# Optimization experiments

Measured on AMD Instinct MI355X. Metric: run time of the kernel, lower is better.

## Reference

```python
import jax, jax.numpy as jnp
import numpy as np

TAIL_BOUND = 3.0
MIN_BIN_W = 1e-3
MIN_BIN_H = 1e-3
MIN_DERIV = 1e-3


def _rq_spline_fwd(x, uw, uh, us):
    # unconstrained rational-quadratic spline (Durkan et al., 'linear' tails)
    # x: [N, C]; uw, uh: [C, B]; us: [C, B-1]
    C, B = uw.shape
    dt = x.dtype
    inside = (x >= -TAIL_BOUND) & (x <= TAIL_BOUND)
    xc = jnp.clip(x, -TAIL_BOUND, TAIL_BOUND)

    widths = MIN_BIN_W + (1.0 - MIN_BIN_W * B) * jax.nn.softmax(uw, axis=-1)
    cumw = jnp.concatenate([jnp.zeros((C, 1), dt), jnp.cumsum(widths, -1)], -1)
    cumw = 2.0 * TAIL_BOUND * cumw - TAIL_BOUND
    cumw = cumw.at[:, 0].set(-TAIL_BOUND).at[:, -1].set(TAIL_BOUND)
    widths = cumw[:, 1:] - cumw[:, :-1]

    heights = MIN_BIN_H + (1.0 - MIN_BIN_H * B) * jax.nn.softmax(uh, axis=-1)
    cumh = jnp.concatenate([jnp.zeros((C, 1), dt), jnp.cumsum(heights, -1)], -1)
    cumh = 2.0 * TAIL_BOUND * cumh - TAIL_BOUND
    cumh = cumh.at[:, 0].set(-TAIL_BOUND).at[:, -1].set(TAIL_BOUND)
    heights = cumh[:, 1:] - cumh[:, :-1]

    # boundary derivative logits -> softplus(const) = 1 - MIN_DERIV
    const = float(np.log(np.expm1(1.0 - MIN_DERIV)))
    ud = jnp.concatenate([jnp.full((C, 1), const, dt), us,
                          jnp.full((C, 1), const, dt)], -1)
    derivs = MIN_DERIV + jax.nn.softplus(ud)  # [C, B+1]

    # searchsorted on bin x-edges (eps shift on last edge, as in reference impl)
    edges = cumw.at[:, -1].add(1e-6)
    idx = jnp.clip(jnp.sum(xc[:, :, None] >= edges[None, :, :], -1) - 1, 0, B - 1)  # [N, C]

    ci = jnp.arange(C)[None, :]
    xk = cumw[ci, idx]
    wk = widths[ci, idx]
    yk = cumh[ci, idx]
    hk = heights[ci, idx]
    dk = derivs[ci, idx]
    dk1 = derivs[ci, idx + 1]
    delta = hk / wk

    theta = (xc - xk) / wk
    t1m = theta * (1.0 - theta)
    num = hk * (delta * theta * theta + dk * t1m)
    den = delta + (dk + dk1 - 2.0 * delta) * t1m
    y = yk + num / den
    dnum = delta * delta * (dk1 * theta * theta + 2.0 * delta * t1m
                            + dk * (1.0 - theta) * (1.0 - theta))
    logdet = jnp.log(dnum) - 2.0 * jnp.log(den)

    # identity (log-det 0) outside the interval
    return jnp.where(inside, y, x), jnp.where(inside, logdet, jnp.zeros_like(logdet))


def setup_inputs() -> dict:
    key = jax.random.key(0)
    ks = jax.random.split(key, 6)
    N, L, C, B = 1000000, 8, 8, 32
    return {
        "x": jax.random.normal(ks[0], (N,), jnp.float32),
        "w": jax.random.normal(ks[1], (L, C, B), jnp.float32),
        "h": jax.random.normal(ks[2], (L, C, B), jnp.float32),
        "s": jax.random.normal(ks[3], (L, C, B - 1), jnp.float32),
        "bias": jax.random.normal(ks[4], (L + 1, C), jnp.float32),
        "log_scale": jax.random.normal(ks[5], (L + 1, C), jnp.float32),
    }


def reference(x, w, h, s, bias, log_scale):
    L, C = w.shape[0], w.shape[1]
    z = jnp.broadcast_to(x[:, None], (x.shape[0], C))
    log_j = jnp.zeros_like(z)
    for step in range(L):
        z = (z - bias[step]) * jnp.exp(-log_scale[step])
        z, ld = _rq_spline_fwd(z, w[step], h[step], s[step])
        log_j = log_j + ld - log_scale[step]
    z = (z - bias[L]) * jnp.exp(-log_scale[L])
    return z, log_j - log_scale[L]
```

## Files before the change

kernel.cpp:

```cpp
#include <hip/hip_runtime.h>
#include <hip/hip_bf16.h>


#define TB 3.0f
#define NB 32
#define NC 8
#define NL 8
#define LN2 0.69314718055994530942f

#define GX0 -6.5f
#define GX1 6.5f
#define TZ 0.5f
#define TL 0.5f

#define PT_FLOATS (64 * 99)
#define GP_FLOATS (PT_FLOATS + 72 + 72 + 8)
#define GP_BYTES  (GP_FLOATS * 4)
#define TAB_OFF   26112
#define CAP 256

__device__ __forceinline__ float softplusf(float v) {
    return fmaxf(v, 0.f) + log1pf(expf(-fabsf(v)));
}

__device__ __forceinline__ unsigned short f2h(float f) {
    _Float16 h = (_Float16)f;
    unsigned short u;
    __builtin_memcpy(&u, &h, 2);
    return u;
}
__device__ __forceinline__ float h2f(unsigned short u) {
    _Float16 h;
    __builtin_memcpy(&h, &u, 2);
    return (float)h;
}

__device__ __forceinline__ int bsearch32(const float* __restrict__ E, float xc) {
    int i = (xc >= E[16]) ? 16 : 0;
    i += (xc >= E[i + 8]) ? 8 : 0;
    i += (xc >= E[i + 4]) ? 4 : 0;
    i += (xc >= E[i + 2]) ? 2 : 0;
    i += (xc >= E[i + 1]) ? 1 : 0;
    return i;
}

__device__ __forceinline__ void spline_eval(const float* __restrict__ Tlc,
                                            float zc, float& zo, float& ldo) {
    const float* E  = Tlc;
    const float* Hc = Tlc + 33;
    const float* Dv = Tlc + 66;

    float xc = fminf(fmaxf(zc, -TB), TB);
    int i = bsearch32(E, xc);

    float xk  = E[i],  xk1 = E[i + 1];
    float yk  = Hc[i], yk1 = Hc[i + 1];
    float dk  = Dv[i], dk1 = Dv[i + 1];

    float wk    = xk1 - xk;
    float hk    = yk1 - yk;
    float invw  = __builtin_amdgcn_rcpf(wk);
    float delta = hk * invw;
    float th    = (xc - xk) * invw;
    float omt   = 1.f - th;
    float t1m   = th * omt;
    float th2   = th * th;

    float num    = hk * fmaf(delta, th2, dk * t1m);
    float den    = fmaf(fmaf(-2.f, delta, dk + dk1), t1m, delta);
    float invden = __builtin_amdgcn_rcpf(den);
    float y      = fmaf(num, invden, yk);

    float dt    = delta * t1m;
    float inner = fmaf(dk1, th2, fmaf(dk, omt * omt, dt + dt));
    float dnum  = (delta * delta) * inner;
    float r  = dnum * invden * invden;
    float ld = LN2 * __builtin_amdgcn_logf(r);

    bool inside = (zc >= -TB) && (zc <= TB);
    zo  = inside ? y : zc;
    ldo = inside ? ld : 0.f;
}

__device__ __forceinline__ void exact_chain(const float* __restrict__ T,
                                            float xv, int c,
                                            float& zout, float& lout) {
    const float* ScT = T + PT_FLOATS;
    const float* BbT = ScT + 72;
    const float* LJT = BbT + 72;
    float zc = xv;
    float lacc = LJT[c];
#pragma unroll 1
    for (int l = 0; l < NL; ++l) {
        zc = (zc - BbT[l * 8 + c]) * ScT[l * 8 + c];
        float ld;
        spline_eval(T + (l * 8 + c) * 99, zc, zc, ld);
        lacc += ld;
    }
    zout = (zc - BbT[NL * 8 + c]) * ScT[NL * 8 + c];
    lout = lacc;
}

extern "C" __global__ void __launch_bounds__(256)
build_tables(const float* __restrict__ w, const float* __restrict__ h,
             const float* __restrict__ s, const float* __restrict__ bias,
             const float* __restrict__ lsc, float* __restrict__ gparam)
{
    __shared__ float T[PT_FLOATS];
    __shared__ float Sc[72], Bb[72], LJ[8];

    const int tid = threadIdx.x;

    if (tid < 64) {
        const int l = tid >> 3, c = tid & 7;
        float* cw = &T[tid * 99];
        const float* wr = w + (l * NC + c) * NB;
        float m = wr[0];
        for (int b = 1; b < NB; ++b) m = fmaxf(m, wr[b]);
        float sum = 0.f;
        for (int b = 0; b < NB; ++b) sum += expf(wr[b] - m);
        float inv = 1.f / sum;
        float acc = 0.f;
        cw[0] = -TB;
        for (int b = 0; b < NB; ++b) {
            acc += 1e-3f + (1.f - 1e-3f * NB) * (expf(wr[b] - m) * inv);
            cw[b + 1] = 6.f * acc - 3.f;
        }
        cw[NB] = TB;
    } else if (tid < 128) {
        const int t = tid - 64;
        float* ch = &T[t * 99 + 33];
        const int l = t >> 3, c = t & 7;
        const float* hr = h + (l * NC + c) * NB;
        float m = hr[0];
        for (int b = 1; b < NB; ++b) m = fmaxf(m, hr[b]);
        float sum = 0.f;
        for (int b = 0; b < NB; ++b) sum += expf(hr[b] - m);
        float inv = 1.f / sum;
        float acc = 0.f;
        ch[0] = -TB;
        for (int b = 0; b < NB; ++b) {
            acc += 1e-3f + (1.f - 1e-3f * NB) * (expf(hr[b] - m) * inv);
            ch[b + 1] = 6.f * acc - 3.f;
        }
        ch[NB] = TB;
    } else if (tid < 192) {
        const int t = tid - 128;
        const int l = t >> 3, c = t & 7;
        float* dv = &T[t * 99 + 66];
        const float* sr = s + (l * NC + c) * (NB - 1);
        const float cst = logf(expm1f(1.f - 1e-3f));
        const float dbound = 1e-3f + softplusf(cst);
        dv[0]  = dbound;
        dv[NB] = dbound;
        for (int k = 0; k < NB - 1; ++k)
            dv[k + 1] = 1e-3f + softplusf(sr[k]);
    }
    if (tid < 72) { Sc[tid] = expf(-lsc[tid]); Bb[tid] = bias[tid]; }
    if (tid < 8) {
        float a = 0.f;
        for (int l = 0; l <= NL; ++l) a += lsc[l * NC + tid];
        LJ[tid] = -a;
    }
    __syncthreads();

    for (int k = tid; k < PT_FLOATS; k += 256) gparam[k] = T[k];
    if (tid < 72) gparam[PT_FLOATS + tid]       = Sc[tid];
    if (tid < 72) gparam[PT_FLOATS + 72 + tid]  = Bb[tid];
    if (tid < 8)  gparam[PT_FLOATS + 144 + tid] = LJ[tid];
}

extern "C" __global__ void __launch_bounds__(256)
grid_eval(const float* __restrict__ gparam, char* __restrict__ tabb,
          int G, float dx)
{
    __shared__ float T[GP_FLOATS];
    __shared__ unsigned short ZL[256 * 16];
    for (int k = threadIdx.x; k < GP_FLOATS; k += 256) T[k] = gparam[k];
    __syncthreads();
    const float* ScT = T + PT_FLOATS;
    const float* BbT = ScT + 72;
    const float* LJT = BbT + 72;

    const int t  = threadIdx.x;
    const int p0 = blockIdx.x * 255;
    const int i  = min(p0 + t, G - 1);

    const float xv = fmaf((float)i, dx, GX0);
    float z[NC], lj[NC];
#pragma unroll
    for (int c = 0; c < NC; ++c) { z[c] = xv; lj[c] = LJT[c]; }

#pragma unroll 1
    for (int l = 0; l < NL; ++l) {
        const float* Tl = T + l * NC * 99;
#pragma unroll
        for (int c = 0; c < NC; ++c) {
            float u = (z[c] - BbT[l * 8 + c]) * ScT[l * 8 + c];
            float zo, ld;
            spline_eval(Tl + c * 99, u, zo, ld);
            z[c] = zo;
            lj[c] += ld;
        }
    }
    unsigned short zh[NC], lh[NC];
#pragma unroll
    for (int c = 0; c < NC; ++c) {
        z[c] = (z[c] - BbT[NL * 8 + c]) * ScT[NL * 8 + c];
        zh[c] = f2h(z[c]);
        lh[c] = f2h(lj[c]);
        ZL[t * 16 + c]     = zh[c];
        ZL[t * 16 + 8 + c] = lh[c];
    }
    __syncthreads();

    const int r = p0 + t;
    if (t < 255 && r <= G - 2) {
        ushort4* rowp = (ushort4*)(tabb + (size_t)r * 64);
#pragma unroll
        for (int c = 0; c < NC; ++c) {
            const float zn  = h2f(ZL[(t + 1) * 16 + c]);
            const float ljn = h2f(ZL[(t + 1) * 16 + 8 + c]);
            ushort4 v;
            v.x = zh[c]; v.y = f2h(zn - h2f(zh[c]));
            v.z = lh[c]; v.w = f2h(ljn - h2f(lh[c]));
            rowp[c] = v;
        }
    }
}

extern "C" __global__ void __launch_bounds__(256)
interp_kernel(const float* __restrict__ x, const char* __restrict__ tabb,
              const float* __restrict__ gparam, float* __restrict__ out,
              int N, int G, float dx, float invdx)
{
    __shared__ float T[GP_FLOATS];
    __shared__ float xbuf[256];
    __shared__ unsigned short pool[CAP];
    __shared__ float resZ[CAP], resL[CAP];
    __shared__ unsigned wgcnt[8][4];

    const int tid   = threadIdx.x;
    const int c     = tid & 7;
    const int pbase = tid >> 3;
    const int lane  = tid & 63;
    const int wloc  = tid >> 6;
    const int P0    = blockIdx.x * 256;

    float zv[8], lv[8], xr[8];
    unsigned long long mg[8];
    unsigned char myf[8];

#pragma unroll
    for (int g = 0; g < 8; ++g) {
        const int pl = g * 32 + pbase;
        const int p  = P0 + pl;
        const bool active = (p < N);
        float xv = 0.f, z0 = 0.f, dz = 0.f, l0 = 0.f, dl = 0.f;
        bool flag = false;
        float t = 0.f;
        if (active) {
            xv = x[p];
            int i = (int)floorf((xv - GX0) * invdx);
            const bool oor = !(xv > GX0 && xv < GX1);
            i = min(max(i, 0), G - 2);
            t = (xv - fmaf((float)i, dx, GX0)) * invdx;
            const uint2 ab = *(const uint2*)(tabb + (size_t)i * 64 + c * 8);
            z0 = h2f((unsigned short)ab.x);
            dz = h2f((unsigned short)(ab.x >> 16));
            l0 = h2f((unsigned short)ab.y);
            dl = h2f((unsigned short)(ab.y >> 16));
            flag = oor || (fabsf(dz) > TZ) || (fabsf(dl) > TL);
        }
        zv[g] = fmaf(t, dz, z0);
        lv[g] = fmaf(t, dl, l0);
        xr[g] = xv;
        myf[g] = flag ? 1 : 0;
        mg[g] = __ballot(flag);
        if (lane == 0) wgcnt[g][wloc] = (unsigned)__popcll(mg[g]);
        if (c == 0) xbuf[pl] = xv;
    }
    __syncthreads();

    unsigned btot = 0;
    unsigned goff[8];
#pragma unroll
    for (int g = 0; g < 8; ++g) {
        unsigned og = btot;
        unsigned wo = 0;
#pragma unroll
        for (int j = 0; j < 4; ++j) {
            const unsigned v = wgcnt[g][j];
            if (j < wloc) wo += v;
            btot += v;
        }
        goff[g] = og + wo;
    }

    const unsigned long long lowmask = (1ull << lane) - 1ull;
#pragma unroll
    for (int g = 0; g < 8; ++g) {
        if (myf[g]) {
            const unsigned idx = goff[g] + (unsigned)__popcll(mg[g] & lowmask);
            if (idx < CAP)
                pool[idx] = (unsigned short)(((g * 32 + pbase) << 3) | c);
        }
    }
    if (btot > 0) {
        for (int k = tid; k < GP_FLOATS; k += 256) T[k] = gparam[k];
    }
    __syncthreads();

    const unsigned pcnt = min(btot, (unsigned)CAP);
    for (unsigned k = tid; k < pcnt; k += 256) {
        const unsigned pr = pool[k];
        float zo, lo;
        exact_chain(T, xbuf[pr >> 3], (int)(pr & 7u), zo, lo);
        resZ[k] = zo; resL[k] = lo;
    }
    __syncthreads();

#pragma unroll
    for (int g = 0; g < 8; ++g) {
        if (myf[g]) {
            const unsigned idx = goff[g] + (unsigned)__popcll(mg[g] & lowmask);
            if (idx < CAP) {
                zv[g] = resZ[idx]; lv[g] = resL[idx];
            } else {
                exact_chain(T, xr[g], c, zv[g], lv[g]);
            }
        }
    }

#pragma unroll
    for (int g = 0; g < 8; ++g) {
        const int pl = g * 32 + pbase;
        const int p  = P0 + pl;
        if (p < N) {
            out[(size_t)p * NC + c] = zv[g];
            out[(size_t)N * NC + (size_t)p * NC + c] = lv[g];
        }
    }
}

extern "C" __global__ void __launch_bounds__(256)
flow_kernel(const float* __restrict__ x, const float* __restrict__ w,
            const float* __restrict__ h, const float* __restrict__ s,
            const float* __restrict__ bias, const float* __restrict__ lsc,
            float* __restrict__ out, int N)
{
    __shared__ float T[PT_FLOATS];
    __shared__ float Bb[NL + 1][NC];
    __shared__ float Sc[NL + 1][NC];
    __shared__ float LJC[NC];

    const int tid = threadIdx.x;
    if (tid < 64) {
        const int l = tid >> 3, c = tid & 7;
        float* cw = &T[tid * 99];
        {
            const float* wr = w + (l * NC + c) * NB;
            float m = wr[0];
            for (int b = 1; b < NB; ++b) m = fmaxf(m, wr[b]);
            float sum = 0.f;
            for (int b = 0; b < NB; ++b) sum += expf(wr[b] - m);
            float inv = 1.f / sum;
            float acc = 0.f;
            cw[0] = -TB;
            for (int b = 0; b < NB; ++b) {
                acc += 1e-3f + (1.f - 1e-3f * NB) * (expf(wr[b] - m) * inv);
                cw[b + 1] = 6.f * acc - 3.f;
            }
            cw[NB] = TB;
        }
        {
            float* ch = cw + 33;
            const float* hr = h + (l * NC + c) * NB;
            float m = hr[0];
            for (int b = 1; b < NB; ++b) m = fmaxf(m, hr[b]);
            float sum = 0.f;
            for (int b = 0; b < NB; ++b) sum += expf(hr[b] - m);
            float inv = 1.f / sum;
            float acc = 0.f;
            ch[0] = -TB;
            for (int b = 0; b < NB; ++b) {
                acc += 1e-3f + (1.f - 1e-3f * NB) * (expf(hr[b] - m) * inv);
                ch[b + 1] = 6.f * acc - 3.f;
            }
            ch[NB] = TB;
        }
        {
            float* dv = cw + 66;
            const float* sr = s + (l * NC + c) * (NB - 1);
            const float cst = logf(expm1f(1.f - 1e-3f));
            const float dbound = 1e-3f + softplusf(cst);
            dv[0]  = dbound;
            dv[NB] = dbound;
            for (int k = 0; k < NB - 1; ++k)
                dv[k + 1] = 1e-3f + softplusf(sr[k]);
        }
    }
    if (tid < (NL + 1) * NC) {
        const int l = tid >> 3, c = tid & 7;
        Bb[l][c] = bias[tid];
        Sc[l][c] = expf(-lsc[tid]);
    }
    if (tid < NC) {
        float a = 0.f;
        for (int l = 0; l <= NL; ++l) a += lsc[l * NC + tid];
        LJC[tid] = -a;
    }
    __syncthreads();

    const int n = blockIdx.x * 256 + tid;
    if (n >= N) return;
    const float xv = x[n];
    float z[NC], lj[NC];
#pragma unroll
    for (int c = 0; c < NC; ++c) { z[c] = xv; lj[c] = LJC[c]; }
#pragma unroll 1
    for (int l = 0; l < NL; ++l) {
        const float* Tl = &T[l * NC * 99];
#pragma unroll
        for (int c = 0; c < NC; ++c) {
            float zc = (z[c] - Bb[l][c]) * Sc[l][c];
            float zo, ld;
            spline_eval(Tl + c * 99, zc, zo, ld);
            z[c] = zo;
            lj[c] += ld;
        }
    }
#pragma unroll
    for (int c = 0; c < NC; ++c) z[c] = (z[c] - Bb[NL][c]) * Sc[NL][c];

    float4* oz = (float4*)(out + (size_t)n * NC);
    oz[0] = make_float4(z[0], z[1], z[2], z[3]);
    oz[1] = make_float4(z[4], z[5], z[6], z[7]);
    float4* ol = (float4*)(out + (size_t)N * NC + (size_t)n * NC);
    ol[0] = make_float4(lj[0], lj[1], lj[2], lj[3]);
    ol[1] = make_float4(lj[4], lj[5], lj[6], lj[7]);
}

extern "C" void kernel_launch(void* const* d_in, const int* in_sizes, int n_in,
                              void* d_out, int out_size, void* d_ws, size_t ws_size,
                              hipStream_t stream) {
    const float* x    = (const float*)d_in[0];
    const float* w    = (const float*)d_in[1];
    const float* h    = (const float*)d_in[2];
    const float* s    = (const float*)d_in[3];
    const float* bias = (const float*)d_in[4];
    const float* lsc  = (const float*)d_in[5];
    float* out = (float*)d_out;
    const int N = in_sizes[0];

    int G = 65536;
    while (G > 2048 && ((size_t)TAB_OFF + (size_t)G * 64) > ws_size)
        G >>= 1;
    const size_t need = (size_t)TAB_OFF + (size_t)G * 64;

    if (need <= ws_size) {
        char* basep = (char*)d_ws;
        float* gparam = (float*)basep;
        char*  tabb   = basep + TAB_OFF;

        const float dx = (GX1 - GX0) / (float)(G - 1);
        const int gblocks = (G - 1 + 254) / 255;
        build_tables<<<1, 256, 0, stream>>>(w, h, s, bias, lsc, gparam);
        grid_eval<<<gblocks, 256, 0, stream>>>(gparam, tabb, G, dx);
        interp_kernel<<<(N + 255) / 256, 256, 0, stream>>>(
            x, tabb, gparam, out, N, G, dx, 1.f / dx);
    } else {
        flow_kernel<<<(N + 255) / 256, 256, 0, stream>>>(
            x, w, h, s, bias, lsc, out, N);
    }
}
```

Measured before the change: 74.61 us.

## Batch table loads up front and compact flagged points per wave

All eight table gathers are now issued before any of their values are used, so global-load latency overlaps instead of being serialized with the interpolation math. Flagged points are compacted into a per-wave pool using a running ballot count rather than a block-wide prefix sum, which removes one barrier and the wgcnt bookkeeping. Unflagged results are written straight to global memory, and exact-chain results are stored directly by the worker thread, so the resZ/resL shared buffers and the final gather pass go away. The cost is the register space for the eight held uint2 loads. Also, each wave now has only 64 pool slots, so a wave with more flagged points sends the extras to a serial per-thread fallback.

```diff
diff --git a/kernel.cpp b/kernel.cpp
--- a/kernel.cpp
+++ b/kernel.cpp
@@ -237,8 +237,7 @@
     __shared__ float T[GP_FLOATS];
     __shared__ float xbuf[256];
     __shared__ unsigned short pool[CAP];
-    __shared__ float resZ[CAP], resL[CAP];
-    __shared__ unsigned wgcnt[8][4];
+    __shared__ unsigned wcnt_lds[4];
 
     const int tid   = threadIdx.x;
     const int c     = tid & 7;
@@ -247,98 +246,99 @@
     const int wloc  = tid >> 6;
     const int P0    = blockIdx.x * 256;
 
-    float zv[8], lv[8], xr[8];
-    unsigned long long mg[8];
-    unsigned char myf[8];
-
+    uint2 ab[8];
+    float xr[8];
 #pragma unroll
     for (int g = 0; g < 8; ++g) {
-        const int pl = g * 32 + pbase;
-        const int p  = P0 + pl;
+        const int p = P0 + g * 32 + pbase;
+        float xv = 0.f;
+        uint2 v; v.x = 0u; v.y = 0u;
+        if (p < N) {
+            xv = x[p];
+            int i = (int)floorf((xv - GX0) * invdx);
+            i = min(max(i, 0), G - 2);
+            v = *(const uint2*)(tabb + (size_t)i * 64 + c * 8);
+        }
+        xr[g] = xv;
+        ab[g] = v;
+        if (c == 0) xbuf[g * 32 + pbase] = xv;
+    }
+
+    unsigned cntw = 0;
+    unsigned ovf  = 0;
+#pragma unroll
+    for (int g = 0; g < 8; ++g) {
+        const int p = P0 + g * 32 + pbase;
         const bool active = (p < N);
-        float xv = 0.f, z0 = 0.f, dz = 0.f, l0 = 0.f, dl = 0.f;
         bool flag = false;
-        float t = 0.f;
+        float zv = 0.f, lv = 0.f;
         if (active) {
-            xv = x[p];
+            const float xv = xr[g];
             int i = (int)floorf((xv - GX0) * invdx);
             const bool oor = !(xv > GX0 && xv < GX1);
             i = min(max(i, 0), G - 2);
-            t = (xv - fmaf((float)i, dx, GX0)) * invdx;
-            const uint2 ab = *(const uint2*)(tabb + (size_t)i * 64 + c * 8);
-            z0 = h2f((unsigned short)ab.x);
-            dz = h2f((unsigned short)(ab.x >> 16));
-            l0 = h2f((unsigned short)ab.y);
-            dl = h2f((unsigned short)(ab.y >> 16));
+            const float t  = (xv - fmaf((float)i, dx, GX0)) * invdx;
+            const float z0 = h2f((unsigned short)ab[g].x);
+            const float dz = h2f((unsigned short)(ab[g].x >> 16));
+            const float l0 = h2f((unsigned short)ab[g].y);
+            const float dl = h2f((unsigned short)(ab[g].y >> 16));
+            zv = fmaf(t, dz, z0);
+            lv = fmaf(t, dl, l0);
             flag = oor || (fabsf(dz) > TZ) || (fabsf(dl) > TL);
         }
-        zv[g] = fmaf(t, dz, z0);
-        lv[g] = fmaf(t, dl, l0);
-        xr[g] = xv;
-        myf[g] = flag ? 1 : 0;
-        mg[g] = __ballot(flag);
-        if (lane == 0) wgcnt[g][wloc] = (unsigned)__popcll(mg[g]);
-        if (c == 0) xbuf[pl] = xv;
-    }
-    __syncthreads();
-
-    unsigned btot = 0;
-    unsigned goff[8];
-#pragma unroll
-    for (int g = 0; g < 8; ++g) {
-        unsigned og = btot;
-        unsigned wo = 0;
-#pragma unroll
-        for (int j = 0; j < 4; ++j) {
-            const unsigned v = wgcnt[g][j];
-            if (j < wloc) wo += v;
-            btot += v;
-        }
-        goff[g] = og + wo;
-    }
-
-    const unsigned long long lowmask = (1ull << lane) - 1ull;
-#pragma unroll
-    for (int g = 0; g < 8; ++g) {
-        if (myf[g]) {
-            const unsigned idx = goff[g] + (unsigned)__popcll(mg[g] & lowmask);
-            if (idx < CAP)
-                pool[idx] = (unsigned short)(((g * 32 + pbase) << 3) | c);
-        }
-    }
+        const unsigned long long m = __ballot(flag);
+        if (flag) {
+            const unsigned rank = cntw +
+                (unsigned)__popcll(m & ((1ull << lane) - 1ull));
+            if (rank < 64u)
+                pool[wloc * 64 + rank] =
+                    (unsigned short)(((g * 32 + pbase) << 3) | c);
+            else
+                ovf |= (1u << g);
+        }
+        cntw += (unsigned)__popcll(m);
+        if (active && !flag) {
+            out[(size_t)p * NC + c] = zv;
+            out[(size_t)N * NC + (size_t)p * NC + c] = lv;
+        }
+    }
+    if (lane == 0) wcnt_lds[wloc] = min(cntw, 64u);
+    __syncthreads();
+
+    const unsigned btot = wcnt_lds[0] + wcnt_lds[1] + wcnt_lds[2] + wcnt_lds[3];
     if (btot > 0) {
         for (int k = tid; k < GP_FLOATS; k += 256) T[k] = gparam[k];
     }
     __syncthreads();
 
-    const unsigned pcnt = min(btot, (unsigned)CAP);
-    for (unsigned k = tid; k < pcnt; k += 256) {
-        const unsigned pr = pool[k];
-        float zo, lo;
-        exact_chain(T, xbuf[pr >> 3], (int)(pr & 7u), zo, lo);
-        resZ[k] = zo; resL[k] = lo;
-    }
-    __syncthreads();
-
-#pragma unroll
-    for (int g = 0; g < 8; ++g) {
-        if (myf[g]) {
-            const unsigned idx = goff[g] + (unsigned)__popcll(mg[g] & lowmask);
-            if (idx < CAP) {
-                zv[g] = resZ[idx]; lv[g] = resL[idx];
-            } else {
-                exact_chain(T, xr[g], c, zv[g], lv[g]);
+    {
+        const unsigned reg = (unsigned)(tid >> 6);
+        const unsigned e   = (unsigned)(tid & 63);
+        if (e < wcnt_lds[reg]) {
+            const unsigned pr = pool[reg * 64 + e];
+            const int pl = (int)(pr >> 3), cc = (int)(pr & 7u);
+            const int p  = P0 + pl;
+            float zo, lo;
+            exact_chain(T, xbuf[pl], cc, zo, lo);
+            if (p < N) {
+                out[(size_t)p * NC + cc] = zo;
+                out[(size_t)N * NC + (size_t)p * NC + cc] = lo;
             }
         }
     }
 
-#pragma unroll
-    for (int g = 0; g < 8; ++g) {
-        const int pl = g * 32 + pbase;
-        const int p  = P0 + pl;
-        if (p < N) {
-            out[(size_t)p * NC + c] = zv[g];
-            out[(size_t)N * NC + (size_t)p * NC + c] = lv[g];
+    if (ovf) {
+#pragma unroll 1
+        for (int g = 0; g < 8; ++g) {
+            if ((ovf >> g) & 1u) {
+                const int p = P0 + g * 32 + pbase;
+                if (p < N) {
+                    float zo, lo;
+                    exact_chain(T, xr[g], c, zo, lo);
+                    out[(size_t)p * NC + c] = zo;
+                    out[(size_t)N * NC + (size_t)p * NC + c] = lo;
+                }
+            }
         }
     }
 }
```

Measured after the change: 73.43 us. No clear change (-1.6%).
